# Performance work log

Hardware: AMD Instinct MI355X
Metric: run time of the kernel (lower is better)

The kernel has to match this reference:

```python
import jax, jax.numpy as jnp
import numpy as np

MARGIN = 0.5

def setup_inputs() -> dict:
    key = jax.random.key(0)
    k1, k2 = jax.random.split(key)
    inputs = jax.random.normal(k1, (8192, 256), dtype=jnp.float32)
    target = jax.random.randint(k2, (8192,), 0, 100, dtype=jnp.int64)
    return {"inputs": inputs, "target": target}

def reference(inputs, target):
    N = inputs.shape[0]
    # pairwise squared distances via ||xi||^2 + ||xj||^2 - 2 xi.xj
    sq = jnp.sum(inputs * inputs, axis=1)  # [N]
    gram = inputs @ inputs.T               # [N, N]
    distance = sq[:, None] + sq[None, :] - 2.0 * gram  # [N, N]
    R = (target[None, :] == target[:, None]).astype(inputs.dtype)  # [N, N]
    loss = R * distance + (1.0 - R) * jnp.maximum(MARGIN - distance, 0.0)
    return jnp.sum(loss) / (N * (N - 1.0) * 2.0)
```

## Files before the change

kernel.cpp:

```cpp
#include <hip/hip_runtime.h>
#include <stdint.h>

#define N      8192
#define KDIM   256
#define BM     128
#define TILES  (N / BM)
#define NPAIRS (TILES * (TILES + 1) / 2)
#define MARGIN 0.5f

typedef float     f32x4 __attribute__((ext_vector_type(4)));
typedef long long i64x2 __attribute__((ext_vector_type(2)));

__device__ __forceinline__ void async_copy16(const void* g, void* l) {
    __builtin_amdgcn_global_load_lds(
        (__attribute__((address_space(1))) void*)(g),
        (__attribute__((address_space(3))) void*)(l),
        16, 0, 0);
}

#if !__has_builtin(__builtin_amdgcn_cvt_pk_fp8_f32)
__device__ __forceinline__ uint32_t f2e4m3(float f) {
    uint32_t u = __float_as_uint(f);
    uint32_t s = (u >> 24) & 0x80u;
    uint32_t au = u & 0x7fffffffu;
    if (au == 0) return s;
    int32_t  exp = (int32_t)(au >> 23) - 127;
    uint32_t man = (au & 0x7fffffu) | 0x800000u;
    uint32_t code;
    if (exp >= -6) {
        code = (uint32_t)((exp + 7) << 3) | ((man >> 20) & 7u);
        uint32_t rem = man & 0xFFFFFu;
        if (rem > 0x80000u || (rem == 0x80000u && (code & 1u))) code++;
    } else {
        int shift = 14 - exp;
        if (shift > 24) return s;
        code = man >> shift;
        uint32_t rem = man & ((1u << shift) - 1u);
        uint32_t h = 1u << (shift - 1);
        if (rem > h || (rem == h && (code & 1u))) code++;
    }
    return s | code;
}
__device__ __forceinline__ uint32_t pack_fp8x4(float4 v) {
    return f2e4m3(v.x) | (f2e4m3(v.y) << 8) | (f2e4m3(v.z) << 16) |
           (f2e4m3(v.w) << 24);
}
#else
__device__ __forceinline__ uint32_t pack_fp8x4(float4 v) {
    int pk = __builtin_amdgcn_cvt_pk_fp8_f32(v.x, v.y, 0, false);
    pk = __builtin_amdgcn_cvt_pk_fp8_f32(v.z, v.w, pk, true);
    return (uint32_t)pk;
}
#endif

__global__ __launch_bounds__(256) void prep_kernel(
        const float* __restrict__ X, uint8_t* __restrict__ Xq,
        float* __restrict__ sq) {
    int row  = blockIdx.x * 4 + (threadIdx.x >> 6);
    int lane = threadIdx.x & 63;

    float4 v = *((const float4*)(X + (size_t)row * KDIM) + lane);
    float ss = v.x * v.x + v.y * v.y + v.z * v.z + v.w * v.w;
    uint32_t pk = pack_fp8x4(v);

    int kg = lane * 4;
    int h  = kg >> 7;
    int kh = kg & 127;
    int ks = kh >> 5;
    int fq = (kh >> 3) & 3;
    int slot = (fq * 2 + (ks >> 1)) ^ (row & 7);
    size_t off = (size_t)row * 256 + h * 128 + slot * 16 + (ks & 1) * 8 + (kh & 4);
    *(uint32_t*)(Xq + off) = pk;

    #pragma unroll
    for (int o = 32; o > 0; o >>= 1) ss += __shfl_down(ss, o, 64);
    if (lane == 0) sq[row] = ss;
}

__global__ __launch_bounds__(256, 4) void loss_kernel(
        const uint8_t* __restrict__ Xq, const float* __restrict__ sq,
        const int* __restrict__ tgt, float* __restrict__ partials) {
    const int p = blockIdx.x;
    float tf = 2.0f * TILES + 1.0f;
    int bi = (int)((tf - sqrtf(tf * tf - 8.0f * (float)p)) * 0.5f);
    if (bi < 0) bi = 0;
    while (bi > 0 && (bi * TILES - bi * (bi - 1) / 2) > p) --bi;
    while (((bi + 1) * TILES - (bi + 1) * bi / 2) <= p) ++bi;
    const int bj = bi + (p - (bi * TILES - bi * (bi - 1) / 2));

    __shared__ __align__(16) uint8_t As[BM * 128];
    __shared__ __align__(16) uint8_t Bs[BM * 128];
    __shared__ float sqa_s[BM], sqb_s[BM];
    __shared__ int   ta_s[BM],  tb_s[BM];
    __shared__ float wsum[4];

    const int tid  = threadIdx.x;
    const int wave = tid >> 6;
    const int lane = tid & 63;

    if (tid < 128) {
        sqa_s[tid] = sq[bi * BM + tid];
        ta_s[tid]  = tgt[bi * BM + tid];
    } else {
        int r = tid - 128;
        sqb_s[r] = sq[bj * BM + r];
        tb_s[r]  = tgt[bj * BM + r];
    }

    const int lrow = lane >> 3;
    const int lb   = (lane & 7) * 16;
    const uint8_t* gA0 = Xq + ((size_t)bi * BM + wave * 32 + lrow) * 256 + lb;
    const uint8_t* gB0 = Xq + ((size_t)bj * BM + wave * 32 + lrow) * 256 + lb;
    uint8_t* lA = As + wave * 32 * 128;
    uint8_t* lB = Bs + wave * 32 * 128;

    const int frow  = lane & 15;
    const int fquad = lane >> 4;
    const int wm = (wave >> 1) * 64;
    const int wn = (wave & 1) * 64;
    const int key = frow & 7;
    const uint8_t* aB = As + (wm + frow) * 128;
    const uint8_t* bB = Bs + (wn + frow) * 128;

    f32x4 acc[4][4];
    #pragma unroll
    for (int im = 0; im < 4; ++im)
        #pragma unroll
        for (int in = 0; in < 4; ++in)
            acc[im][in] = (f32x4){0.f, 0.f, 0.f, 0.f};

    #pragma unroll
    for (int h = 0; h < 2; ++h) {
        #pragma unroll
        for (int q = 0; q < 4; ++q) {
            async_copy16(gA0 + h * 128 + q * 8 * 256, lA + q * 1024);
            async_copy16(gB0 + h * 128 + q * 8 * 256, lB + q * 1024);
        }
        __syncthreads();

        #pragma unroll
        for (int ks2 = 0; ks2 < 2; ++ks2) {
            const int t = ((fquad * 2 + ks2) ^ key) * 16;
            i64x2 a2[4], b2[4];
            #pragma unroll
            for (int im = 0; im < 4; ++im)
                a2[im] = *(const i64x2*)(aB + im * 16 * 128 + t);
            #pragma unroll
            for (int in = 0; in < 4; ++in)
                b2[in] = *(const i64x2*)(bB + in * 16 * 128 + t);
            #pragma unroll
            for (int im = 0; im < 4; ++im)
                #pragma unroll
                for (int in = 0; in < 4; ++in)
                    acc[im][in] = __builtin_amdgcn_mfma_f32_16x16x32_fp8_fp8(
                        a2[im].x, b2[in].x, acc[im][in], 0, 0, 0);
            #pragma unroll
            for (int im = 0; im < 4; ++im)
                #pragma unroll
                for (int in = 0; in < 4; ++in)
                    acc[im][in] = __builtin_amdgcn_mfma_f32_16x16x32_fp8_fp8(
                        a2[im].y, b2[in].y, acc[im][in], 0, 0, 0);
        }
        if (h == 0) __syncthreads();
    }

    float lsum = 0.0f;
    if (bi != bj) {
        #pragma unroll
        for (int im = 0; im < 4; ++im) {
            #pragma unroll
            for (int in = 0; in < 4; ++in) {
                #pragma unroll
                for (int r = 0; r < 4; ++r) {
                    int rl = wm + im * 16 + fquad * 4 + r;
                    int cl = wn + in * 16 + frow;
                    float d = fmaf(-2.0f, acc[im][in][r],
                                   sqa_s[rl] + sqb_s[cl]);
                    lsum += (ta_s[rl] == tb_s[cl]) ? d
                                                   : fmaxf(MARGIN - d, 0.0f);
                }
            }
        }
        lsum *= 2.0f;
    } else {
        #pragma unroll
        for (int im = 0; im < 4; ++im) {
            #pragma unroll
            for (int in = 0; in < 4; ++in) {
                #pragma unroll
                for (int r = 0; r < 4; ++r) {
                    int rl = wm + im * 16 + fquad * 4 + r;
                    int cl = wn + in * 16 + frow;
                    float d = fmaf(-2.0f, acc[im][in][r],
                                   sqa_s[rl] + sqb_s[cl]);
                    float c = (ta_s[rl] == tb_s[cl]) ? d
                                                     : fmaxf(MARGIN - d, 0.0f);
                    float w = (rl < cl) ? 2.0f : ((rl == cl) ? 1.0f : 0.0f);
                    lsum += w * c;
                }
            }
        }
    }

    #pragma unroll
    for (int o = 32; o > 0; o >>= 1) lsum += __shfl_down(lsum, o, 64);
    if (lane == 0) wsum[wave] = lsum;
    __syncthreads();
    if (tid == 0) partials[p] = wsum[0] + wsum[1] + wsum[2] + wsum[3];
}

__global__ __launch_bounds__(256) void reduce_kernel(
        const float* __restrict__ partials, float* __restrict__ out,
        int n, float scale) {
    float s = 0.0f;
    for (int i = threadIdx.x; i < n; i += 256) s += partials[i];
    __shared__ float w[4];
    #pragma unroll
    for (int o = 32; o > 0; o >>= 1) s += __shfl_down(s, o, 64);
    int wave = threadIdx.x >> 6, lane = threadIdx.x & 63;
    if (lane == 0) w[wave] = s;
    __syncthreads();
    if (threadIdx.x == 0) out[0] = (w[0] + w[1] + w[2] + w[3]) * scale;
}

extern "C" void kernel_launch(void* const* d_in, const int* in_sizes, int n_in,
                              void* d_out, int out_size, void* d_ws, size_t ws_size,
                              hipStream_t stream) {
    (void)in_sizes; (void)n_in; (void)out_size; (void)ws_size;
    const float* X   = (const float*)d_in[0];
    const int*   tgt = (const int*)d_in[1];

    uint8_t* Xq     = (uint8_t*)d_ws;
    float* sq       = (float*)((char*)d_ws + (size_t)N * KDIM);
    float* partials = sq + N;

    prep_kernel<<<N / 4, 256, 0, stream>>>(X, Xq, sq);
    loss_kernel<<<NPAIRS, 256, 0, stream>>>(Xq, sq, tgt, partials);

    const float scale = (float)(1.0 / ((double)N * ((double)N - 1.0) * 2.0));
    reduce_kernel<<<1, 256, 0, stream>>>(partials, (float*)d_out, NPAIRS, scale);
}
```

Measured before the change: 80.74 us.

## Use MI355 scaled 16x16x128 FP8 MFMA with matching K-layout in prep

Replaces the 16x16x32 FP8 MFMA sequence (four K-steps per half) with a single gfx950 mfma_scale_f32_16x16x128_f8f6f4 per output tile per half, using unit scales. The prep kernel's swizzled fp8 layout is rewritten so each lane reads two 16-byte chunks that form the 32-byte K slice the new instruction expects. This cuts the MFMA instruction count and register shuffling, but the epilogue, the sqrt-based pair indexing and the unpipelined loads stay unchanged, and the kernel as a whole may be dominated by those.

```diff
diff --git a/kernel.cpp b/kernel.cpp
--- a/kernel.cpp
+++ b/kernel.cpp
@@ -7,9 +7,11 @@
 #define TILES  (N / BM)
 #define NPAIRS (TILES * (TILES + 1) / 2)
 #define MARGIN 0.5f
-
-typedef float     f32x4 __attribute__((ext_vector_type(4)));
-typedef long long i64x2 __attribute__((ext_vector_type(2)));
+#define SCALE1 0x7f7f7f7f
+
+typedef float f32x4 __attribute__((ext_vector_type(4)));
+typedef int   i32x4 __attribute__((ext_vector_type(4)));
+typedef int   i32x8 __attribute__((ext_vector_type(8)));
 
 __device__ __forceinline__ void async_copy16(const void* g, void* l) {
     __builtin_amdgcn_global_load_lds(
@@ -63,14 +65,10 @@
     float ss = v.x * v.x + v.y * v.y + v.z * v.z + v.w * v.w;
     uint32_t pk = pack_fp8x4(v);
 
-    int kg = lane * 4;
-    int h  = kg >> 7;
-    int kh = kg & 127;
-    int ks = kh >> 5;
-    int fq = (kh >> 3) & 3;
-    int slot = (fq * 2 + (ks >> 1)) ^ (row & 7);
-    size_t off = (size_t)row * 256 + h * 128 + slot * 16 + (ks & 1) * 8 + (kh & 4);
-    *(uint32_t*)(Xq + off) = pk;
+    int h   = lane >> 5;
+    int g   = (lane >> 2) & 7;
+    int pos = g ^ (row & 7);
+    *(uint32_t*)(Xq + (size_t)row * 256 + h * 128 + pos * 16 + (lane & 3) * 4) = pk;
 
     #pragma unroll
     for (int o = 32; o > 0; o >>= 1) ss += __shfl_down(ss, o, 64);
@@ -109,8 +107,8 @@
 
     const int lrow = lane >> 3;
     const int lb   = (lane & 7) * 16;
-    const uint8_t* gA0 = Xq + ((size_t)bi * BM + wave * 32 + lrow) * 256 + lb;
-    const uint8_t* gB0 = Xq + ((size_t)bj * BM + wave * 32 + lrow) * 256 + lb;
+    const uint8_t* gA = Xq + ((size_t)bi * BM + wave * 32 + lrow) * 256 + lb;
+    const uint8_t* gB = Xq + ((size_t)bj * BM + wave * 32 + lrow) * 256 + lb;
     uint8_t* lA = As + wave * 32 * 128;
     uint8_t* lB = Bs + wave * 32 * 128;
 
@@ -118,9 +116,11 @@
     const int fquad = lane >> 4;
     const int wm = (wave >> 1) * 64;
     const int wn = (wave & 1) * 64;
-    const int key = frow & 7;
-    const uint8_t* aB = As + (wm + frow) * 128;
-    const uint8_t* bB = Bs + (wn + frow) * 128;
+    const int key  = frow & 7;
+    const int off0 = ((fquad * 2 + 0) ^ key) * 16;
+    const int off1 = ((fquad * 2 + 1) ^ key) * 16;
+    const uint8_t* aBp = As + (wm + frow) * 128;
+    const uint8_t* bBp = Bs + (wn + frow) * 128;
 
     f32x4 acc[4][4];
     #pragma unroll
@@ -133,33 +133,28 @@
     for (int h = 0; h < 2; ++h) {
         #pragma unroll
         for (int q = 0; q < 4; ++q) {
-            async_copy16(gA0 + h * 128 + q * 8 * 256, lA + q * 1024);
-            async_copy16(gB0 + h * 128 + q * 8 * 256, lB + q * 1024);
+            async_copy16(gA + h * 128 + q * 8 * 256, lA + q * 1024);
+            async_copy16(gB + h * 128 + q * 8 * 256, lB + q * 1024);
         }
         __syncthreads();
 
-        #pragma unroll
-        for (int ks2 = 0; ks2 < 2; ++ks2) {
-            const int t = ((fquad * 2 + ks2) ^ key) * 16;
-            i64x2 a2[4], b2[4];
+        i32x8 a8[4];
+        #pragma unroll
+        for (int im = 0; im < 4; ++im) {
+            i32x4 al = *(const i32x4*)(aBp + im * 16 * 128 + off0);
+            i32x4 ah = *(const i32x4*)(aBp + im * 16 * 128 + off1);
+            a8[im] = __builtin_shufflevector(al, ah, 0, 1, 2, 3, 4, 5, 6, 7);
+        }
+        #pragma unroll
+        for (int in = 0; in < 4; ++in) {
+            i32x4 bl = *(const i32x4*)(bBp + in * 16 * 128 + off0);
+            i32x4 bh = *(const i32x4*)(bBp + in * 16 * 128 + off1);
+            i32x8 b8 = __builtin_shufflevector(bl, bh, 0, 1, 2, 3, 4, 5, 6, 7);
             #pragma unroll
             for (int im = 0; im < 4; ++im)
-                a2[im] = *(const i64x2*)(aB + im * 16 * 128 + t);
-            #pragma unroll
-            for (int in = 0; in < 4; ++in)
-                b2[in] = *(const i64x2*)(bB + in * 16 * 128 + t);
-            #pragma unroll
-            for (int im = 0; im < 4; ++im)
-                #pragma unroll
-                for (int in = 0; in < 4; ++in)
-                    acc[im][in] = __builtin_amdgcn_mfma_f32_16x16x32_fp8_fp8(
-                        a2[im].x, b2[in].x, acc[im][in], 0, 0, 0);
-            #pragma unroll
-            for (int im = 0; im < 4; ++im)
-                #pragma unroll
-                for (int in = 0; in < 4; ++in)
-                    acc[im][in] = __builtin_amdgcn_mfma_f32_16x16x32_fp8_fp8(
-                        a2[im].y, b2[in].y, acc[im][in], 0, 0, 0);
+                acc[im][in] = __builtin_amdgcn_mfma_scale_f32_16x16x128_f8f6f4(
+                    a8[im], b8, acc[im][in], 0, 0,
+                    0, SCALE1, 0, SCALE1);
         }
         if (h == 0) __syncthreads();
     }
```

Measured after the change: 81.51 us. No clear change (+1.0%).
